# Kernel optimization log

Hardware: AMD Instinct MI355X
Metric: run time of the kernel (lower is better)

The kernel has to match this reference:

```python
import jax, jax.numpy as jnp
import numpy as np

D_MODEL = 768
N_HEADS = 12
D_HEAD = D_MODEL // N_HEADS


def setup_inputs() -> dict:
    key = jax.random.key(0)
    k_x, k_qw, k_qb, k_ow, k_ob = jax.random.split(key, 5)
    B, N = 2, 4096
    scale = 1.0 / np.sqrt(D_MODEL)
    return {
        "x": jax.random.normal(k_x, (B, N, D_MODEL), dtype=jnp.float32),
        # torch nn.Linear stores weight as [out_features, in_features]
        "qkv_w": jax.random.uniform(k_qw, (3 * D_MODEL, D_MODEL), jnp.float32, -scale, scale),
        "qkv_b": jax.random.uniform(k_qb, (3 * D_MODEL,), jnp.float32, -scale, scale),
        "out_w": jax.random.uniform(k_ow, (D_MODEL, D_MODEL), jnp.float32, -scale, scale),
        "out_b": jax.random.uniform(k_ob, (D_MODEL,), jnp.float32, -scale, scale),
    }


def reference(x, qkv_w, qkv_b, out_w, out_b):
    B, N, D = x.shape
    qkv = x @ qkv_w.T + qkv_b                                   # [B, N, 3D]
    qkv = qkv.reshape(B, N, 3, N_HEADS, D_HEAD)
    qkv = jnp.transpose(qkv, (2, 0, 3, 1, 4))                    # [3, B, H, N, d]
    q, k, v = qkv[0], qkv[1], qkv[2]
    scores = jnp.einsum("bhqd,bhkd->bhqk", q, k) / np.sqrt(D_HEAD)
    attn = jax.nn.softmax(scores, axis=-1)
    out = jnp.einsum("bhqk,bhkd->bhqd", attn, v)                 # [B, H, N, d]
    out = jnp.transpose(out, (0, 2, 1, 3)).reshape(B, N, D)
    return out @ out_w.T + out_b
```

## Files before the change

kernel.cpp:

```cpp
#include <hip/hip_runtime.h>
#include <cstdint>

#define SEQ 4096
#define NH 12
#define DH 64
#define DM 768
#define MT 8192
#define QKVN 2304
#define BH 24

typedef __bf16 bf16;
typedef __attribute__((ext_vector_type(8))) __bf16 bf16x8;
typedef __attribute__((ext_vector_type(4))) __bf16 bf16x4;
typedef __attribute__((ext_vector_type(2))) __bf16 bf16x2;
typedef __attribute__((ext_vector_type(4))) float f32x4;
typedef __attribute__((ext_vector_type(16))) float f32x16;
typedef __attribute__((ext_vector_type(2))) int int2v;

__device__ __forceinline__ void async_ld16(const void* g, void* lds) {
  __builtin_amdgcn_global_load_lds(
      (__attribute__((address_space(1))) void*)(void*)g,
      (__attribute__((address_space(3))) void*)lds, 16, 0, 0);
}

__device__ __forceinline__ int sexp2_bits(float s) {
  return (int)__builtin_fmaf(s, 8388608.0f, 1065091072.0f);
}

__device__ __forceinline__ int pack_hi16(int lo, int hi) {
#if __has_builtin(__builtin_amdgcn_perm)
  return (int)__builtin_amdgcn_perm((unsigned)hi, (unsigned)lo, 0x07060302u);
#else
  return (int)(((unsigned)lo >> 16) | ((unsigned)hi & 0xffff0000u));
#endif
}

__device__ __forceinline__ void lane32_swap(int& a, int& b) {
#if __has_builtin(__builtin_amdgcn_permlane32_swap)
  int2v r = __builtin_amdgcn_permlane32_swap(a, b, false, false);
  a = r.x; b = r.y;
#else
  int hi = (threadIdx.x & 63) >> 5;
  int ra = __shfl_xor(a, 32, 64), rb = __shfl_xor(b, 32, 64);
  int na = hi ? rb : a;
  int nb = hi ? b : ra;
  a = na; b = nb;
#endif
}

#define NX4  (MT * DM / 4)
#define NW14 (QKVN * DM / 4)
#define NW24 (DM * DM / 4)
__global__ void cvt_all(const float* __restrict__ x, const float* __restrict__ w1,
                        const float* __restrict__ w2, bf16* __restrict__ xb,
                        bf16* __restrict__ wb1, bf16* __restrict__ wb2) {
  int i = blockIdx.x * blockDim.x + threadIdx.x;
  const float* src; bf16* dst; int j;
  if (i < NX4) { src = x; dst = xb; j = i; }
  else if (i < NX4 + NW14) { src = w1; dst = wb1; j = i - NX4; }
  else if (i < NX4 + NW14 + NW24) { src = w2; dst = wb2; j = i - NX4 - NW14; }
  else return;
  f32x4 v = ((const f32x4*)src)[j];
  bf16x4 o;
  o.x = (bf16)v.x; o.y = (bf16)v.y; o.z = (bf16)v.z; o.w = (bf16)v.w;
  ((bf16x4*)dst)[j] = o;
}

template<int MODE>
__global__ __launch_bounds__(256) void gemm_bt(
    const bf16* __restrict__ A, const bf16* __restrict__ Bw,
    const float* __restrict__ bias,
    bf16* __restrict__ outQ, bf16* __restrict__ outK, bf16* __restrict__ outVt,
    float* __restrict__ outF,
    int M, int N, int K)
{
  __shared__ bf16 smem[2 * 128 * 64];
  bf16* sA = smem;
  bf16* sB = smem + 128 * 64;
  bf16* sT = smem;

  const int tid  = threadIdx.x;
  const int wave = tid >> 6;
  const int lane = tid & 63;
  const int l15  = lane & 15;
  const int quad = lane >> 4;

  constexpr int NT = (MODE == 0) ? (QKVN / 128) : (DM / 128);
  const int lin = blockIdx.x;
  const int rem = lin % (NT * 8);
  const int m0 = ((lin / (NT * 8)) * 8 + (rem % 8)) * 128;
  const int n0 = (rem / 8) * 128;

  const int rowbase = (wave >> 1) * 64;
  const int colbase = (wave & 1) * 64;

  f32x4 acc[4][4] = {};

  const int srow = lane >> 3;
  const int spg  = (lane & 7) ^ srow;
  const int xk   = l15 & 7;

  for (int kt = 0; kt < K; kt += 64) {
#pragma unroll
    for (int p = 0; p < 8; ++p) {
      int chunk = p * 4 + wave;
      if (chunk < 16) {
        int row = chunk * 8 + srow;
        async_ld16(A + (size_t)(m0 + row) * K + kt + spg * 8, &sA[chunk * 512]);
      } else {
        int row = (chunk - 16) * 8 + srow;
        async_ld16(Bw + (size_t)(n0 + row) * K + kt + spg * 8, &sB[(chunk - 16) * 512]);
      }
    }
    __syncthreads();

#pragma unroll
    for (int ks = 0; ks < 2; ++ks) {
      bf16x8 af[4], bfr[4];
#pragma unroll
      for (int rt = 0; rt < 4; ++rt)
        af[rt] = *(const bf16x8*)&sA[(rowbase + rt * 16 + l15) * 64 +
                                     (((ks * 4 + quad) ^ xk) * 8)];
#pragma unroll
      for (int ct = 0; ct < 4; ++ct)
        bfr[ct] = *(const bf16x8*)&sB[(colbase + ct * 16 + l15) * 64 +
                                      (((ks * 4 + quad) ^ xk) * 8)];
#pragma unroll
      for (int rt = 0; rt < 4; ++rt)
#pragma unroll
        for (int ct = 0; ct < 4; ++ct)
          acc[rt][ct] = __builtin_amdgcn_mfma_f32_16x16x32_bf16(af[rt], bfr[ct], acc[rt][ct], 0, 0, 0);
    }
    __syncthreads();
  }

  if (MODE == 0) {
    const int g = n0 / DM;
    if (g < 2) {
      const float qscale = 0.125f * 1.4426950408889634f;
#pragma unroll
      for (int ct = 0; ct < 4; ++ct) {
        int j = n0 + colbase + ct * 16 + l15;
        float bj = bias[j];
        int f = j % DM;
        int h = f >> 6, d = f & 63;
#pragma unroll
        for (int rt = 0; rt < 4; ++rt) {
          int mrow = m0 + rowbase + rt * 16 + quad * 4;
#pragma unroll
          for (int r = 0; r < 4; ++r) {
            float v = acc[rt][ct][r] + bj;
            int m = mrow + r;
            int b = m >> 12, n = m & 4095;
            int bh = b * NH + h;
            if (g == 0) outQ[((size_t)bh * SEQ + n) * DH + d] = (bf16)(v * qscale);
            else        outK[((size_t)bh * SEQ + n) * DH + d] = (bf16)v;
          }
        }
      }
    } else {
      const int f0 = n0 - 2 * DM;
      const int b = m0 >> 12, n0m = m0 & 4095;
#pragma unroll
      for (int p = 0; p < 2; ++p) {
        __syncthreads();
        if (colbase == p * 64) {
#pragma unroll
          for (int ct = 0; ct < 4; ++ct) {
            int jl = ct * 16 + l15;
            float bj = bias[n0 + p * 64 + jl];
#pragma unroll
            for (int rt = 0; rt < 4; ++rt) {
              int ml = rowbase + rt * 16 + quad * 4;
#pragma unroll
              for (int r = 0; r < 4; ++r)
                sT[jl * 136 + ml + r] = (bf16)(acc[rt][ct][r] + bj);
            }
          }
        }
        __syncthreads();
#pragma unroll
        for (int p2 = 0; p2 < 4; ++p2) {
          int slot = p2 * 256 + tid;
          int jr = slot >> 4, mc = (slot & 15) * 8;
          int fj = f0 + p * 64 + jr;
          int h = fj >> 6, d = fj & 63;
          *(bf16x8*)&outVt[((size_t)(b * NH + h) * DH + d) * SEQ + n0m + mc] =
              *(const bf16x8*)&sT[jr * 136 + mc];
        }
      }
    }
  } else {
#pragma unroll
    for (int ct = 0; ct < 4; ++ct) {
      int j = n0 + colbase + ct * 16 + l15;
      float bj = bias[j];
#pragma unroll
      for (int rt = 0; rt < 4; ++rt) {
        int mrow = m0 + rowbase + rt * 16 + quad * 4;
#pragma unroll
        for (int r = 0; r < 4; ++r)
          outF[(size_t)(mrow + r) * N + j] = acc[rt][ct][r] + bj;
      }
    }
  }
}

#define SOFTPV(S, R0, R1, R2, R3, OA, OB) do {                               \
    int b0 = sexp2_bits(S[8*kc+0]); int b1 = sexp2_bits(S[8*kc+1]);          \
    int b2 = sexp2_bits(S[8*kc+2]); int b3 = sexp2_bits(S[8*kc+3]);          \
    int b4 = sexp2_bits(S[8*kc+4]); int b5 = sexp2_bits(S[8*kc+5]);          \
    int b6 = sexp2_bits(S[8*kc+6]); int b7 = sexp2_bits(S[8*kc+7]);          \
    R0 += __int_as_float(b0 & 0xffff0000) + __int_as_float(b4 & 0xffff0000); \
    R1 += __int_as_float(b1 & 0xffff0000) + __int_as_float(b5 & 0xffff0000); \
    R2 += __int_as_float(b2 & 0xffff0000) + __int_as_float(b6 & 0xffff0000); \
    R3 += __int_as_float(b3 & 0xffff0000) + __int_as_float(b7 & 0xffff0000); \
    int g0a = pack_hi16(b0, b1), g0b = pack_hi16(b2, b3);                    \
    int g1a = pack_hi16(b4, b5), g1b = pack_hi16(b6, b7);                    \
    lane32_swap(g0a, g1a); lane32_swap(g0b, g1b);                            \
    union { int i[4]; bf16x8 v; } Af_;                                       \
    Af_.i[0] = g0a; Af_.i[1] = g0b; Af_.i[2] = g1a; Af_.i[3] = g1b;          \
    OA = __builtin_amdgcn_mfma_f32_32x32x16_bf16(Af_.v, vf0, OA, 0, 0, 0);   \
    OB = __builtin_amdgcn_mfma_f32_32x32x16_bf16(Af_.v, vf1, OB, 0, 0, 0);   \
  } while (0)

template<int SPLIT>
__global__ __launch_bounds__(256, 2) void flash_attn(
    const bf16* __restrict__ Q, const bf16* __restrict__ Kg,
    const bf16* __restrict__ Vt, float* __restrict__ Op,
    float* __restrict__ Rs, bf16* __restrict__ Oout)
{
  __shared__ bf16 sK[2][64 * 64];
  __shared__ bf16 sV[2][64 * 64];

  int bh, qb, kh;
  if (SPLIT) {
    const int L    = blockIdx.x + 32 * blockIdx.y;
    const int slot = L >> 3;
    bh = (L & 7) + 8 * (slot >> 5);
    qb = (slot & 31) >> 1;
    kh = slot & 1;
  } else {
    const int L    = blockIdx.x + 16 * blockIdx.y;
    const int slot = L >> 3;
    bh = (L & 7) + 8 * (slot >> 4);
    qb = slot & 15;
    kh = 0;
  }

  {
    int ph = (qb + bh + kh) & 3;
    if (ph == 1) __builtin_amdgcn_s_sleep(2);
    else if (ph == 2) __builtin_amdgcn_s_sleep(4);
    else if (ph == 3) __builtin_amdgcn_s_sleep(6);
  }

  const int tid  = threadIdx.x;
  const int wave = tid >> 6;
  const int lane = tid & 63;
  const int l31  = lane & 31;
  const int hi   = lane >> 5;
  const int q0w  = qb * 256 + wave * 64;
  const int kbase = SPLIT ? kh * (SEQ / 2) : 0;
  const int kend  = SPLIT ? kbase + SEQ / 2 : SEQ;

  const bf16* Qb = Q  + (size_t)bh * SEQ * DH;
  const bf16* Kb = Kg + (size_t)bh * SEQ * DH;
  const bf16* Vb = Vt + (size_t)bh * DH * SEQ;

  const int srow = lane >> 3;
  const int spg  = lane & 7;

  bf16x8 qf0[4], qf1[4];
#pragma unroll
  for (int dc = 0; dc < 4; ++dc) {
    qf0[dc] = *(const bf16x8*)&Qb[(size_t)(q0w + l31) * DH + dc * 16 + hi * 8];
    qf1[dc] = *(const bf16x8*)&Qb[(size_t)(q0w + 32 + l31) * DH + dc * 16 + hi * 8];
  }

  f32x16 o00 = {}, o01 = {}, o10 = {}, o11 = {};
  const f32x16 zc = {};
  float r00 = 0.f, r01 = 0.f, r02 = 0.f, r03 = 0.f;
  float r10 = 0.f, r11 = 0.f, r12 = 0.f, r13 = 0.f;

  const int keyk = (l31 & 7) ^ (((l31 >> 3) & 3) << 1);
  int off[4];
#pragma unroll
  for (int dc = 0; dc < 4; ++dc)
    off[dc] = l31 * 64 + (((dc * 2 + hi) ^ keyk) * 8);

  auto stage = [&](int kt, int buf) {
#pragma unroll
    for (int j = 0; j < 2; ++j) {
      int r0 = wave * 16 + j * 8;
      int row = r0 + srow;
      int lg = spg ^ (row & 7) ^ (((row >> 3) & 3) << 1);
      async_ld16(Kb + (size_t)(kt + row) * DH + lg * 8, &sK[buf][r0 * 64]);
      async_ld16(Vb + (size_t)row * SEQ + kt + lg * 8, &sV[buf][r0 * 64]);
    }
  };

  auto compute = [&](const bf16* sKp, const bf16* sVp) {
#pragma unroll
    for (int kb = 0; kb < 2; ++kb) {
      bf16x8 kf[4];
#pragma unroll
      for (int dc = 0; dc < 4; ++dc)
        kf[dc] = *(const bf16x8*)&sKp[off[dc] + kb * 2048];
      f32x16 s0 = __builtin_amdgcn_mfma_f32_32x32x16_bf16(kf[0], qf0[0], zc, 0, 0, 0);
      f32x16 s1 = __builtin_amdgcn_mfma_f32_32x32x16_bf16(kf[0], qf1[0], zc, 0, 0, 0);
#pragma unroll
      for (int dc = 1; dc < 4; ++dc) {
        s0 = __builtin_amdgcn_mfma_f32_32x32x16_bf16(kf[dc], qf0[dc], s0, 0, 0, 0);
        s1 = __builtin_amdgcn_mfma_f32_32x32x16_bf16(kf[dc], qf1[dc], s1, 0, 0, 0);
      }
#pragma unroll
      for (int kc = 0; kc < 2; ++kc) {
        bf16x8 vf0 = *(const bf16x8*)&sVp[off[kb * 2 + kc]];
        bf16x8 vf1 = *(const bf16x8*)&sVp[off[kb * 2 + kc] + 2048];
        SOFTPV(s0, r00, r01, r02, r03, o00, o01);
        SOFTPV(s1, r10, r11, r12, r13, o10, o11);
      }
    }
  };

  stage(kbase, 0);
  __syncthreads();

  for (int kt = kbase; kt < kend; kt += 128) {
    if (kt + 64 < kend) stage(kt + 64, 1);
    compute(sK[0], sV[0]);
    __syncthreads();
    if (kt + 128 < kend) stage(kt + 128, 0);
    compute(sK[1], sV[1]);
    __syncthreads();
  }

  float rsum0 = (r00 + r01) + (r02 + r03);
  rsum0 += __shfl_xor(rsum0, 32, 64);
  float rsum1 = (r10 + r11) + (r12 + r13);
  rsum1 += __shfl_xor(rsum1, 32, 64);

  if (SPLIT) {
    float* Oh = Op + ((size_t)(kh * BH + bh) * SEQ + q0w) * DH;
    if (hi == 0) {
      float* Rh = Rs + (size_t)(kh * BH + bh) * SEQ + q0w;
      Rh[l31]      = rsum0;
      Rh[32 + l31] = rsum1;
    }
#pragma unroll
    for (int i = 0; i < 16; ++i) {
      int ql = 8 * (i >> 2) + (i & 3) + 4 * hi;
      Oh[(size_t)ql * DH + l31]             = o00[i];
      Oh[(size_t)ql * DH + 32 + l31]        = o01[i];
      Oh[(size_t)(32 + ql) * DH + l31]      = o10[i];
      Oh[(size_t)(32 + ql) * DH + 32 + l31] = o11[i];
    }
  } else {
    float inv0 = 1.0f / rsum0;
    float inv1 = 1.0f / rsum1;
    const int bg = bh / NH, h = bh % NH;
#pragma unroll
    for (int i = 0; i < 16; ++i) {
      int ql = 8 * (i >> 2) + (i & 3) + 4 * hi;
      float iva = __shfl(inv0, ql, 64);
      size_t basea = (size_t)(bg * SEQ + q0w + ql) * DM + h * DH;
      Oout[basea + l31]      = (bf16)(o00[i] * iva);
      Oout[basea + 32 + l31] = (bf16)(o01[i] * iva);
      float ivb = __shfl(inv1, ql, 64);
      size_t baseb = (size_t)(bg * SEQ + q0w + 32 + ql) * DM + h * DH;
      Oout[baseb + l31]      = (bf16)(o10[i] * ivb);
      Oout[baseb + 32 + l31] = (bf16)(o11[i] * ivb);
    }
  }
}

__global__ __launch_bounds__(256) void merge_halves(
    const float* __restrict__ Op, const float* __restrict__ Rs,
    bf16* __restrict__ attnV)
{
  int i = blockIdx.x * 256 + threadIdx.x;
  if (i >= BH * SEQ * (DH / 4)) return;
  int dq = i & 15, row = i >> 4;
  f32x4 a = ((const f32x4*)Op)[(size_t)row * 16 + dq];
  f32x4 b = ((const f32x4*)Op)[((size_t)BH * SEQ + row) * 16 + dq];
  float inv = 1.0f / (Rs[row] + Rs[BH * SEQ + row]);
  int q = row & (SEQ - 1), bh = row >> 12;
  int bg = bh / NH, h = bh % NH;
  bf16x4 r;
  r.x = (bf16)((a.x + b.x) * inv);
  r.y = (bf16)((a.y + b.y) * inv);
  r.z = (bf16)((a.z + b.z) * inv);
  r.w = (bf16)((a.w + b.w) * inv);
  *(bf16x4*)&attnV[((size_t)(bg * SEQ + q)) * DM + h * DH + dq * 4] = r;
}

extern "C" void kernel_launch(void* const* d_in, const int* in_sizes, int n_in,
                              void* d_out, int out_size, void* d_ws, size_t ws_size,
                              hipStream_t stream) {
  const float* x     = (const float*)d_in[0];
  const float* qkv_w = (const float*)d_in[1];
  const float* qkv_b = (const float*)d_in[2];
  const float* out_w = (const float*)d_in[3];
  const float* out_b = (const float*)d_in[4];
  float* out = (float*)d_out;

  char* w = (char*)d_ws;
  bf16* xb    = (bf16*)w; w += (size_t)MT * DM * 2;
  bf16* wqkv  = (bf16*)w; w += (size_t)QKVN * DM * 2;
  bf16* wout  = (bf16*)w; w += (size_t)DM * DM * 2;
  bf16* Qw    = (bf16*)w; w += (size_t)MT * DM * 2;
  bf16* Kw    = (bf16*)w; w += (size_t)MT * DM * 2;
  bf16* Vtw   = (bf16*)w; w += (size_t)MT * DM * 2;
  bf16* attnV = (bf16*)w; w += (size_t)MT * DM * 2;
  float* Opf  = (float*)w; w += (size_t)2 * BH * SEQ * DH * 4;
  float* Rsf  = (float*)w; w += (size_t)2 * BH * SEQ * 4;
  const size_t ws_need = (size_t)(w - (char*)d_ws);

  const int tot4 = NX4 + NW14 + NW24;
  cvt_all<<<dim3((tot4 + 255) / 256), 256, 0, stream>>>(x, qkv_w, out_w, xb, wqkv, wout);

  gemm_bt<0><<<dim3((QKVN / 128) * (MT / 128)), 256, 0, stream>>>(
      xb, wqkv, qkv_b, Qw, Kw, Vtw, nullptr, MT, QKVN, DM);

  if (ws_size >= ws_need) {
    flash_attn<1><<<dim3(32, BH), 256, 0, stream>>>(Qw, Kw, Vtw, Opf, Rsf, nullptr);
    merge_halves<<<dim3(BH * SEQ * (DH / 4) / 256), 256, 0, stream>>>(Opf, Rsf, attnV);
  } else {
    flash_attn<0><<<dim3(16, BH), 256, 0, stream>>>(Qw, Kw, Vtw, nullptr, nullptr, attnV);
  }

  gemm_bt<1><<<dim3((DM / 128) * (MT / 128)), 256, 0, stream>>>(
      attnV, wout, out_b, nullptr, nullptr, nullptr, out, MT, DM, DM);
}
```

Measured before the change: 265.4 us.

## Fuse split-attention merge into output GEMM and coalesce Q/K epilogue stores

Removes the merge_halves kernel by loading the two fp32 partial attention outputs and row sums directly in the output projection GEMM, normalizing and converting to bf16 while filling shared memory. Also restages the Q/K projection epilogue through shared memory so it writes 16-byte coalesced vectors instead of scattered scalar bf16 stores. The fused GEMM re-reads the fp32 partials once per output column tile and uses synchronous loads, which raises memory traffic compared with reading a bf16 intermediate.

```diff
diff --git a/kernel.cpp b/kernel.cpp
--- a/kernel.cpp
+++ b/kernel.cpp
@@ -137,25 +137,36 @@
   if (MODE == 0) {
     const int g = n0 / DM;
     if (g < 2) {
-      const float qscale = 0.125f * 1.4426950408889634f;
-#pragma unroll
-      for (int ct = 0; ct < 4; ++ct) {
-        int j = n0 + colbase + ct * 16 + l15;
-        float bj = bias[j];
-        int f = j % DM;
-        int h = f >> 6, d = f & 63;
-#pragma unroll
-        for (int rt = 0; rt < 4; ++rt) {
-          int mrow = m0 + rowbase + rt * 16 + quad * 4;
-#pragma unroll
-          for (int r = 0; r < 4; ++r) {
-            float v = acc[rt][ct][r] + bj;
-            int m = mrow + r;
-            int b = m >> 12, n = m & 4095;
-            int bh = b * NH + h;
-            if (g == 0) outQ[((size_t)bh * SEQ + n) * DH + d] = (bf16)(v * qscale);
-            else        outK[((size_t)bh * SEQ + n) * DH + d] = (bf16)v;
+      const float sc = (g == 0) ? 0.125f * 1.4426950408889634f : 1.0f;
+      bf16* outQK = (g == 0) ? outQ : outK;
+      const int f0q = n0 - g * DM;
+      const int b = m0 >> 12, n0m = m0 & 4095;
+#pragma unroll
+      for (int p = 0; p < 2; ++p) {
+        __syncthreads();
+        if (colbase == p * 64) {
+#pragma unroll
+          for (int ct = 0; ct < 4; ++ct) {
+            int c = ct * 16 + l15;
+            float bj = bias[n0 + p * 64 + c];
+#pragma unroll
+            for (int rt = 0; rt < 4; ++rt) {
+              int ml = rowbase + rt * 16 + quad * 4;
+#pragma unroll
+              for (int r = 0; r < 4; ++r)
+                sT[(ml + r) * 72 + c] = (bf16)((acc[rt][ct][r] + bj) * sc);
+            }
           }
+        }
+        __syncthreads();
+        const int h = (f0q + p * 64) >> 6;
+        const int bh = b * NH + h;
+#pragma unroll
+        for (int p2 = 0; p2 < 4; ++p2) {
+          int slot = p2 * 256 + tid;
+          int mr = slot >> 3, cg = slot & 7;
+          *(bf16x8*)&outQK[((size_t)bh * SEQ + n0m + mr) * DH + cg * 8] =
+              *(const bf16x8*)&sT[mr * 72 + cg * 8];
         }
       }
     } else {
@@ -202,6 +213,102 @@
         for (int r = 0; r < 4; ++r)
           outF[(size_t)(mrow + r) * N + j] = acc[rt][ct][r] + bj;
       }
+    }
+  }
+}
+
+__global__ __launch_bounds__(256) void gemm_out_fused(
+    const float* __restrict__ Op, const float* __restrict__ Rs,
+    const bf16* __restrict__ Bw, const float* __restrict__ bias,
+    float* __restrict__ outF)
+{
+  __shared__ bf16 smem[2 * 128 * 64];
+  bf16* sA = smem;
+  bf16* sB = smem + 128 * 64;
+
+  const int tid  = threadIdx.x;
+  const int wave = tid >> 6;
+  const int lane = tid & 63;
+  const int l15  = lane & 15;
+  const int quad = lane >> 4;
+
+  const int lin = blockIdx.x;
+  const int rem = lin % 48;
+  const int m0 = ((lin / 48) * 8 + (rem % 8)) * 128;
+  const int n0 = (rem / 8) * 128;
+
+  const int rowbase = (wave >> 1) * 64;
+  const int colbase = (wave & 1) * 64;
+
+  f32x4 acc[4][4] = {};
+
+  const int srow = lane >> 3;
+  const int spg  = (lane & 7) ^ srow;
+  const int xk   = l15 & 7;
+  const int arow = wave * 8 + (lane >> 3);
+  const int gd   = lane & 7;
+
+  for (int kt = 0; kt < DM; kt += 64) {
+    const int h = kt >> 6;
+#pragma unroll
+    for (int p = 0; p < 4; ++p) {
+      int chunk = p * 4 + wave;
+      int row = chunk * 8 + srow;
+      async_ld16(Bw + (size_t)(n0 + row) * DM + kt + spg * 8, &sB[chunk * 512]);
+    }
+#pragma unroll
+    for (int s = 0; s < 4; ++s) {
+      int row = s * 32 + arow;
+      int m = m0 + row;
+      int bg = m >> 12, q = m & 4095;
+      size_t rbase = (size_t)(bg * NH + h) * SEQ + q;
+      const float* p0 = Op + rbase * DH + gd * 8;
+      const float* p1 = p0 + (size_t)BH * SEQ * DH;
+      f32x4 x0 = *(const f32x4*)p0;
+      f32x4 x1 = *(const f32x4*)(p0 + 4);
+      f32x4 y0 = *(const f32x4*)p1;
+      f32x4 y1 = *(const f32x4*)(p1 + 4);
+      float inv = 1.0f / (Rs[rbase] + Rs[(size_t)BH * SEQ + rbase]);
+      bf16x8 o;
+#pragma unroll
+      for (int j = 0; j < 4; ++j) {
+        o[j]     = (bf16)((x0[j] + y0[j]) * inv);
+        o[4 + j] = (bf16)((x1[j] + y1[j]) * inv);
+      }
+      *(bf16x8*)&sA[row * 64 + (gd ^ (row & 7)) * 8] = o;
+    }
+    __syncthreads();
+
+#pragma unroll
+    for (int ks = 0; ks < 2; ++ks) {
+      bf16x8 af[4], bfr[4];
+#pragma unroll
+      for (int rt = 0; rt < 4; ++rt)
+        af[rt] = *(const bf16x8*)&sA[(rowbase + rt * 16 + l15) * 64 +
+                                     (((ks * 4 + quad) ^ xk) * 8)];
+#pragma unroll
+      for (int ct = 0; ct < 4; ++ct)
+        bfr[ct] = *(const bf16x8*)&sB[(colbase + ct * 16 + l15) * 64 +
+                                      (((ks * 4 + quad) ^ xk) * 8)];
+#pragma unroll
+      for (int rt = 0; rt < 4; ++rt)
+#pragma unroll
+        for (int ct = 0; ct < 4; ++ct)
+          acc[rt][ct] = __builtin_amdgcn_mfma_f32_16x16x32_bf16(af[rt], bfr[ct], acc[rt][ct], 0, 0, 0);
+    }
+    __syncthreads();
+  }
+
+#pragma unroll
+  for (int ct = 0; ct < 4; ++ct) {
+    int j = n0 + colbase + ct * 16 + l15;
+    float bj = bias[j];
+#pragma unroll
+    for (int rt = 0; rt < 4; ++rt) {
+      int mrow = m0 + rowbase + rt * 16 + quad * 4;
+#pragma unroll
+      for (int r = 0; r < 4; ++r)
+        outF[(size_t)(mrow + r) * DM + j] = acc[rt][ct][r] + bj;
     }
   }
 }
@@ -375,26 +482,6 @@
   }
 }
 
-__global__ __launch_bounds__(256) void merge_halves(
-    const float* __restrict__ Op, const float* __restrict__ Rs,
-    bf16* __restrict__ attnV)
-{
-  int i = blockIdx.x * 256 + threadIdx.x;
-  if (i >= BH * SEQ * (DH / 4)) return;
-  int dq = i & 15, row = i >> 4;
-  f32x4 a = ((const f32x4*)Op)[(size_t)row * 16 + dq];
-  f32x4 b = ((const f32x4*)Op)[((size_t)BH * SEQ + row) * 16 + dq];
-  float inv = 1.0f / (Rs[row] + Rs[BH * SEQ + row]);
-  int q = row & (SEQ - 1), bh = row >> 12;
-  int bg = bh / NH, h = bh % NH;
-  bf16x4 r;
-  r.x = (bf16)((a.x + b.x) * inv);
-  r.y = (bf16)((a.y + b.y) * inv);
-  r.z = (bf16)((a.z + b.z) * inv);
-  r.w = (bf16)((a.w + b.w) * inv);
-  *(bf16x4*)&attnV[((size_t)(bg * SEQ + q)) * DM + h * DH + dq * 4] = r;
-}
-
 extern "C" void kernel_launch(void* const* d_in, const int* in_sizes, int n_in,
                               void* d_out, int out_size, void* d_ws, size_t ws_size,
                               hipStream_t stream) {
@@ -425,11 +512,11 @@
 
   if (ws_size >= ws_need) {
     flash_attn<1><<<dim3(32, BH), 256, 0, stream>>>(Qw, Kw, Vtw, Opf, Rsf, nullptr);
-    merge_halves<<<dim3(BH * SEQ * (DH / 4) / 256), 256, 0, stream>>>(Opf, Rsf, attnV);
+    gemm_out_fused<<<dim3((DM / 128) * (MT / 128)), 256, 0, stream>>>(
+        Opf, Rsf, wout, out_b, out);
   } else {
     flash_attn<0><<<dim3(16, BH), 256, 0, stream>>>(Qw, Kw, Vtw, nullptr, nullptr, attnV);
-  }
-
-  gemm_bt<1><<<dim3((DM / 128) * (MT / 128)), 256, 0, stream>>>(
-      attnV, wout, out_b, nullptr, nullptr, nullptr, out, MT, DM, DM);
-}
+    gemm_bt<1><<<dim3((DM / 128) * (MT / 128)), 256, 0, stream>>>(
+        attnV, wout, out_b, nullptr, nullptr, nullptr, out, MT, DM, DM);
+  }
+}
```

After: 275.2 us. 1.04x slower.

## Stage Q/K epilogue through LDS for coalesced 16-byte stores and remap block order

Applied to the files above, without the earlier changes.

The Q and K outputs of the QKV GEMM were written as scattered 2-byte stores per accumulator element. They are now staged through shared memory in two 64-column passes and written as coalesced 16-byte vector stores per head row, mirroring the existing V path. The block index is also permuted so consecutive blocks are spread across the rasterized tile order, which may improve cache locality or balance across XCDs. The cost is extra LDS traffic and barriers in the epilogue.

```diff
diff --git a/kernel.cpp b/kernel.cpp
--- a/kernel.cpp
+++ b/kernel.cpp
@@ -86,9 +86,11 @@
   const int quad = lane >> 4;
 
   constexpr int NT = (MODE == 0) ? (QKVN / 128) : (DM / 128);
+  constexpr int CPX = NT * 8;
   const int lin = blockIdx.x;
-  const int rem = lin % (NT * 8);
-  const int m0 = ((lin / (NT * 8)) * 8 + (rem % 8)) * 128;
+  const int v   = (lin & 7) * CPX + (lin >> 3);
+  const int rem = v % CPX;
+  const int m0 = ((v / CPX) * 8 + (rem % 8)) * 128;
   const int n0 = (rem / 8) * 128;
 
   const int rowbase = (wave >> 1) * 64;
@@ -137,25 +139,36 @@
   if (MODE == 0) {
     const int g = n0 / DM;
     if (g < 2) {
-      const float qscale = 0.125f * 1.4426950408889634f;
-#pragma unroll
-      for (int ct = 0; ct < 4; ++ct) {
-        int j = n0 + colbase + ct * 16 + l15;
-        float bj = bias[j];
-        int f = j % DM;
-        int h = f >> 6, d = f & 63;
-#pragma unroll
-        for (int rt = 0; rt < 4; ++rt) {
-          int mrow = m0 + rowbase + rt * 16 + quad * 4;
-#pragma unroll
-          for (int r = 0; r < 4; ++r) {
-            float v = acc[rt][ct][r] + bj;
-            int m = mrow + r;
-            int b = m >> 12, n = m & 4095;
-            int bh = b * NH + h;
-            if (g == 0) outQ[((size_t)bh * SEQ + n) * DH + d] = (bf16)(v * qscale);
-            else        outK[((size_t)bh * SEQ + n) * DH + d] = (bf16)v;
+      const float sc = (g == 0) ? 0.125f * 1.4426950408889634f : 1.0f;
+      bf16* outQK = (g == 0) ? outQ : outK;
+      const int f0q = n0 - g * DM;
+      const int b = m0 >> 12, n0m = m0 & 4095;
+#pragma unroll
+      for (int p = 0; p < 2; ++p) {
+        __syncthreads();
+        if (colbase == p * 64) {
+#pragma unroll
+          for (int ct = 0; ct < 4; ++ct) {
+            int c = ct * 16 + l15;
+            float bj = bias[n0 + p * 64 + c];
+#pragma unroll
+            for (int rt = 0; rt < 4; ++rt) {
+              int ml = rowbase + rt * 16 + quad * 4;
+#pragma unroll
+              for (int r = 0; r < 4; ++r)
+                sT[(ml + r) * 72 + c] = (bf16)((acc[rt][ct][r] + bj) * sc);
+            }
           }
+        }
+        __syncthreads();
+        const int h = (f0q + p * 64) >> 6;
+        const int bh = b * NH + h;
+#pragma unroll
+        for (int p2 = 0; p2 < 4; ++p2) {
+          int slot = p2 * 256 + tid;
+          int mr = slot >> 3, cg = slot & 7;
+          *(bf16x8*)&outQK[((size_t)bh * SEQ + n0m + mr) * DH + cg * 8] =
+              *(const bf16x8*)&sT[mr * 72 + cg * 8];
         }
       }
     } else {
```

Measured after the change: 266.0 us. About the same (+0.2%).
